# Performance work log

Hardware: AMD Instinct MI355X
Metric: run time of the kernel (lower is better)

The kernel has to match this reference:

```python
import jax, jax.numpy as jnp
import numpy as np

N = 100000      # nodes
E = 3200000     # edges (avg degree 32)
NODE, EDGE, H = 11, 2, 32
EPS = 1e-5


def setup_inputs() -> dict:
    key = jax.random.key(0)
    ks = jax.random.split(key, 12)
    def w(k, shape):  # small init like torch Linear
        return jax.random.normal(k, shape, dtype=jnp.float32) * 0.1
    inp = {
        'x': jax.random.normal(ks[0], (N, NODE), dtype=jnp.float32),
        'edge_attr': jax.random.normal(ks[1], (E, EDGE), dtype=jnp.float32),
        'edge_index': jax.random.randint(ks[2], (2, E), 0, N),
        # mlp1: Lin(13,32)-BN-ReLU-Lin(32,32)-BN-ReLU
        'w1a': w(ks[3], (NODE + EDGE, H)), 'b1a': jnp.zeros(H), 'g1a': jnp.ones(H), 'be1a': jnp.zeros(H),
        'w1b': w(ks[4], (H, H)),           'b1b': jnp.zeros(H), 'g1b': jnp.ones(H), 'be1b': jnp.zeros(H),
        # mlp2: Lin(43,32)-BN-ReLU then Lin(32,1)-ReLU (no BN on last)
        'w2a': w(ks[5], (NODE + H, H)), 'b2a': jnp.zeros(H), 'g2a': jnp.ones(H), 'be2a': jnp.zeros(H),
        'w2b': w(ks[6], (H, 1)),        'b2b': jnp.zeros(1),
        # power: Lin(11,32)-BN-ReLU-Lin(32,1)-BN-ReLU
        'wpa': w(ks[7], (NODE, H)), 'bpa': jnp.zeros(H), 'gpa': jnp.ones(H), 'bepa': jnp.zeros(H),
        'wpb': w(ks[8], (H, 1)),    'bpb': jnp.zeros(1), 'gpb': jnp.ones(1), 'bepb': jnp.zeros(1),
    }
    return inp


def _bn(x, g, b):
    # training-mode BatchNorm1d (batch stats, biased variance), like torch default
    mu = x.mean(0, keepdims=True)
    var = ((x - mu) ** 2).mean(0, keepdims=True)
    return (x - mu) * jax.lax.rsqrt(var + EPS) * g + b


def _conv(x, edge_index, edge_attr,
          w1a, b1a, g1a, be1a, w1b, b1b, g1b, be1b,
          w2a, b2a, g2a, be2a, w2b, b2b):
    src, dst = edge_index[0], edge_index[1]
    # message: cat([x_j, edge_attr]) -> mlp1
    m = jnp.concatenate([x[src], edge_attr], axis=1)          # [E, 13]
    m = jax.nn.relu(_bn(m @ w1a + b1a, g1a, be1a))            # [E, 32]
    m = jax.nn.relu(_bn(m @ w1b + b1b, g1b, be1b))            # [E, 32]
    # aggr='max' scatter to destination nodes
    agg = jax.ops.segment_max(m, dst, num_segments=x.shape[0])
    agg = jnp.where(jnp.isneginf(agg), 0.0, agg)              # empty segments -> 0
    # update: cat([x, aggr_out]) -> mlp2, then replace last feature column
    h = jax.nn.relu(_bn(jnp.concatenate([x, agg], axis=1) @ w2a + b2a, g2a, be2a))
    comb = jax.nn.relu(h @ w2b + b2b)                         # [N, 1]
    return jnp.concatenate([x[:, :-1], comb], axis=1)         # [N, 11]


def reference(x, edge_attr, edge_index,
              w1a, b1a, g1a, be1a, w1b, b1b, g1b, be1b,
              w2a, b2a, g2a, be2a, w2b, b2b,
              wpa, bpa, gpa, bepa, wpb, bpb, gpb, bepb):
    for _ in range(3):
        x = _conv(x, edge_index, edge_attr,
                  w1a, b1a, g1a, be1a, w1b, b1b, g1b, be1b,
                  w2a, b2a, g2a, be2a, w2b, b2b)
    h = jax.nn.relu(_bn(x @ wpa + bpa, gpa, bepa))
    out = jax.nn.relu(_bn(h @ wpb + bpb, gpb, bepb))
    return out
```

## Files before the change

kernel.cpp:

```cpp
#include <hip/hip_runtime.h>
#include <hip/hip_bf16.h>
#include <cstddef>

#define NN 100000
#define EE 3200000
#define NBIN 64
static const float EF = 3200000.0f;


__device__ __forceinline__ float wsum(float v) {
  #pragma unroll
  for (int off = 32; off > 0; off >>= 1) v += __shfl_down(v, off, 64);
  return v;
}

__device__ __forceinline__ void reduce64(float sum[32], float ssq[32], float* red,
                                         float* __restrict__ gsum, float* __restrict__ gssq) {
  const int wid = threadIdx.x >> 6, lane = threadIdx.x & 63;
  #pragma unroll
  for (int j = 0; j < 32; j++) {
    float a = wsum(sum[j]);
    float b = wsum(ssq[j]);
    if (lane == 0) { red[wid * 64 + j] = a; red[wid * 64 + 32 + j] = b; }
  }
  __syncthreads();
  if (threadIdx.x < 64) {
    float t = red[threadIdx.x] + red[64 + threadIdx.x] + red[128 + threadIdx.x] + red[192 + threadIdx.x];
    if (threadIdx.x < 32) unsafeAtomicAdd(&gsum[threadIdx.x], t);
    else                  unsafeAtomicAdd(&gssq[threadIdx.x - 32], t);
  }
}

__device__ __forceinline__ void loadrow(const float* __restrict__ xp, int s, float in[13]) {
  const float4* xr = reinterpret_cast<const float4*>(xp + (size_t)s * 12);
  float4 r0 = xr[0], r1 = xr[1], r2 = xr[2];
  in[0]=r0.x; in[1]=r0.y; in[2]=r0.z; in[3]=r0.w; in[4]=r1.x; in[5]=r1.y; in[6]=r1.z; in[7]=r1.w;
  in[8]=r2.x; in[9]=r2.y; in[10]=r2.z;
}


__global__ __launch_bounds__(256) void k_wprep(const float* __restrict__ w1b,
    const float* __restrict__ b1b, const float* __restrict__ g1b,
    const float* __restrict__ w2a, const float* __restrict__ b2a,
    const float* __restrict__ wpa, const float* __restrict__ bpa,
    float* __restrict__ w2tf, float* __restrict__ b1bf,
    float* __restrict__ w2aT, float* __restrict__ wpaT) {
  int t = threadIdx.x;
  for (int i = t; i < 1024; i += 256) {
    int j = i >> 5, k = i & 31;
    float d = (g1b[j] >= 0.f) ? 1.f : -1.f;
    w2tf[j * 32 + k] = d * w1b[k * 32 + j];
  }
  for (int i = t; i < 32 * 43; i += 256) { int j = i & 31, k = i >> 5; w2aT[j * 44 + k] = w2a[k * 32 + j]; }
  for (int i = t; i < 32 * 11; i += 256) { int j = i & 31, k = i >> 5; wpaT[j * 12 + k] = wpa[k * 32 + j]; }
  if (t < 32) {
    float d = (g1b[t] >= 0.f) ? 1.f : -1.f;
    b1bf[t] = d * b1b[t];
    w2aT[t * 44 + 43] = b2a[t];
    wpaT[t * 12 + 11] = bpa[t];
  }
}

__global__ __launch_bounds__(256) void k_prep(const int* __restrict__ dst, const int* __restrict__ src,
    const float* __restrict__ ea, int* __restrict__ cnt, int* __restrict__ rank,
    float* __restrict__ nsd, float* __restrict__ cmom) {
  float p0 = 0, p1 = 0, p2 = 0, p3 = 0, p4 = 0;
  const int S = gridDim.x * 256;
  for (int g = blockIdx.x * 256 + threadIdx.x; g < EE / 4; g += S) {
    int4 d4 = reinterpret_cast<const int4*>(dst)[g];
    int4 s4 = reinterpret_cast<const int4*>(src)[g];
    float4 e0 = reinterpret_cast<const float4*>(ea)[2 * g];
    float4 e1 = reinterpret_cast<const float4*>(ea)[2 * g + 1];
    int r0 = atomicAdd(&cnt[d4.x], 1);
    int r1 = atomicAdd(&cnt[d4.y], 1);
    int r2 = atomicAdd(&cnt[d4.z], 1);
    int r3 = atomicAdd(&cnt[d4.w], 1);
    reinterpret_cast<int4*>(rank)[g] = make_int4(r0, r1, r2, r3);
    atomicAdd(reinterpret_cast<int*>(&nsd[4 * s4.x]), 1);
    unsafeAtomicAdd(&nsd[4 * s4.x + 1], e0.x); unsafeAtomicAdd(&nsd[4 * s4.x + 2], e0.y);
    atomicAdd(reinterpret_cast<int*>(&nsd[4 * s4.y]), 1);
    unsafeAtomicAdd(&nsd[4 * s4.y + 1], e0.z); unsafeAtomicAdd(&nsd[4 * s4.y + 2], e0.w);
    atomicAdd(reinterpret_cast<int*>(&nsd[4 * s4.z]), 1);
    unsafeAtomicAdd(&nsd[4 * s4.z + 1], e1.x); unsafeAtomicAdd(&nsd[4 * s4.z + 2], e1.y);
    atomicAdd(reinterpret_cast<int*>(&nsd[4 * s4.w]), 1);
    unsafeAtomicAdd(&nsd[4 * s4.w + 1], e1.z); unsafeAtomicAdd(&nsd[4 * s4.w + 2], e1.w);
    p0 += e0.x * e0.x + e0.z * e0.z + e1.x * e1.x + e1.z * e1.z;
    p1 += e0.x * e0.y + e0.z * e0.w + e1.x * e1.y + e1.z * e1.w;
    p2 += e0.y * e0.y + e0.w * e0.w + e1.y * e1.y + e1.w * e1.w;
    p3 += e0.x + e0.z + e1.x + e1.z;
    p4 += e0.y + e0.w + e1.y + e1.w;
  }
  p0 = wsum(p0); p1 = wsum(p1); p2 = wsum(p2); p3 = wsum(p3); p4 = wsum(p4);
  if ((threadIdx.x & 63) == 0) {
    unsafeAtomicAdd(&cmom[0], p0); unsafeAtomicAdd(&cmom[1], p1); unsafeAtomicAdd(&cmom[2], p2);
    unsafeAtomicAdd(&cmom[3], p3); unsafeAtomicAdd(&cmom[4], p4);
  }
}

__global__ __launch_bounds__(1024) void k_scan(const int* __restrict__ cnt,
                                               int* __restrict__ starts) {
  __shared__ int part[1024];
  const int T = 1024, CH = (NN + T - 1) / T;
  int t = threadIdx.x;
  int lo = t * CH, hi = min(lo + CH, NN);
  int s = 0;
  for (int i = lo; i < hi; i++) s += cnt[i];
  part[t] = s; __syncthreads();
  for (int off = 1; off < T; off <<= 1) {
    int v = (t >= off) ? part[t - off] : 0;
    __syncthreads();
    part[t] += v;
    __syncthreads();
  }
  int run = part[t] - s;
  for (int i = lo; i < hi; i++) { starts[i] = run; run += cnt[i]; }
  if (t == T - 1) starts[NN] = EE;
}

__global__ __launch_bounds__(256) void k_scatter(const int* __restrict__ dst, const int* __restrict__ src,
    const float* __restrict__ ea, const int* __restrict__ starts, const int* __restrict__ rank,
    int4* __restrict__ edg) {
  const int S = gridDim.x * 256;
  for (int g = blockIdx.x * 256 + threadIdx.x; g < EE / 4; g += S) {
    int4 d4 = reinterpret_cast<const int4*>(dst)[g];
    int4 s4 = reinterpret_cast<const int4*>(src)[g];
    int4 r4 = reinterpret_cast<const int4*>(rank)[g];
    float4 e0 = reinterpret_cast<const float4*>(ea)[2 * g];
    float4 e1 = reinterpret_cast<const float4*>(ea)[2 * g + 1];
    edg[starts[d4.x] + r4.x] = make_int4(s4.x, __float_as_int(e0.x), __float_as_int(e0.y), 0);
    edg[starts[d4.y] + r4.y] = make_int4(s4.y, __float_as_int(e0.z), __float_as_int(e0.w), 0);
    edg[starts[d4.z] + r4.z] = make_int4(s4.z, __float_as_int(e1.x), __float_as_int(e1.y), 0);
    edg[starts[d4.w] + r4.w] = make_int4(s4.w, __float_as_int(e1.z), __float_as_int(e1.w), 0);
  }
}

__global__ __launch_bounds__(256) void k_xp(const float* __restrict__ x, float* __restrict__ xp) {
  int n = blockIdx.x * 256 + threadIdx.x;
  if (n >= NN) return;
  float v[11];
  #pragma unroll
  for (int k = 0; k < 11; k++) v[k] = x[(size_t)n * 11 + k];
  float4* o = reinterpret_cast<float4*>(xp + (size_t)n * 12);
  o[0] = make_float4(v[0], v[1], v[2], v[3]);
  o[1] = make_float4(v[4], v[5], v[6], v[7]);
  o[2] = make_float4(v[8], v[9], v[10], 0.f);
}

__global__ __launch_bounds__(256) void k_mom(const float* __restrict__ xp, const float* __restrict__ nsd,
                                             float* __restrict__ mom) {
  const int n = blockIdx.x * 256 + threadIdx.x;
  const int lane = threadIdx.x & 63;
  float v[11]; float w = 0.f; float sx = 0.f, sy = 0.f;
  #pragma unroll
  for (int k = 0; k < 11; k++) v[k] = 0.f;
  if (n < NN) {
    float4 nv = reinterpret_cast<const float4*>(nsd)[n];
    w = (float)__float_as_int(nv.x);
    sx = nv.y; sy = nv.z;
    loadrow(xp, n, v);
  }
  int ch = 0;
  #pragma unroll
  for (int a = 0; a < 11; a++) {
    float r = wsum(w * v[a]);
    if (lane == 0) unsafeAtomicAdd(&mom[ch], r);
    ch++;
  }
  #pragma unroll
  for (int a = 0; a < 11; a++) {
    #pragma unroll
    for (int b = a; b < 11; b++) {
      float r = wsum(w * v[a] * v[b]);
      if (lane == 0) unsafeAtomicAdd(&mom[ch], r);
      ch++;
    }
  }
  #pragma unroll
  for (int a = 0; a < 11; a++) {
    float rx = wsum(v[a] * sx);
    if (lane == 0) unsafeAtomicAdd(&mom[ch], rx);
    ch++;
    float ry = wsum(v[a] * sy);
    if (lane == 0) unsafeAtomicAdd(&mom[ch], ry);
    ch++;
  }
}

__device__ __forceinline__ float msym(const float* mom, const float* cmom, int k, int l) {
  int a = min(k, l), b = max(k, l);
  if (b < 11) return mom[11 + a * 11 - a * (a - 1) / 2 + (b - a)];
  if (a < 11) return mom[77 + a * 2 + (b - 11)];
  return cmom[(a - 11) + (b - 11)];
}

__global__ void k_fin1(float* __restrict__ mom, const float* __restrict__ cmom,
    const float* __restrict__ w1a, const float* __restrict__ b1a,
    const float* __restrict__ g1a, const float* __restrict__ be1a,
    float* __restrict__ w1f, float* __restrict__ wexy) {
  int j = threadIdx.x;
  float w[13], S[13];
  #pragma unroll
  for (int k = 0; k < 13; k++) w[k] = w1a[k * 32 + j];
  #pragma unroll
  for (int k = 0; k < 11; k++) S[k] = mom[k];
  S[11] = cmom[3]; S[12] = cmom[4];
  float lin = 0.f;
  #pragma unroll
  for (int k = 0; k < 13; k++) lin = fmaf(w[k], S[k], lin);
  float quad = 0.f;
  #pragma unroll
  for (int k = 0; k < 13; k++)
    #pragma unroll
    for (int l = 0; l < 13; l++) quad = fmaf(w[k] * w[l], msym(mom, cmom, k, l), quad);
  const float invE = 1.f / EF;
  float b = b1a[j];
  float mean = fmaf(lin, invE, b);
  float ey2 = (quad + 2.f * b * lin) * invE + b * b;
  float var = fmaxf(ey2 - mean * mean, 0.f);
  float A = g1a[j] * rsqrtf(var + 1e-5f);
  float C = be1a[j] - mean * A;
  #pragma unroll
  for (int k = 0; k < 13; k++) w1f[j * 16 + k] = A * w[k];
  w1f[j * 16 + 13] = fmaf(A, b, C);
  w1f[j * 16 + 14] = 0.f; w1f[j * 16 + 15] = 0.f;
  wexy[j] = A * w[11];
  wexy[32 + j] = A * w[12];
  __syncthreads();
  for (int i = j; i < 128; i += 32) mom[i] = 0.f;
}

__global__ __launch_bounds__(256) void k_P(const float* __restrict__ xp, const float* __restrict__ w1f,
                                           float* __restrict__ P) {
  const int n = blockIdx.x * 256 + threadIdx.x;
  if (n >= NN) return;
  float xv[11];
  loadrow(xp, n, xv);
  float4* op = reinterpret_cast<float4*>(P + (size_t)n * 32);
  #pragma unroll
  for (int jj = 0; jj < 8; jj++) {
    float o[4];
    #pragma unroll
    for (int u = 0; u < 4; u++) {
      int j = 4 * jj + u;
      const float* wr = w1f + j * 16;
      float acc = wr[13];
      #pragma unroll
      for (int k = 0; k < 11; k++) acc = fmaf(xv[k], wr[k], acc);
      o[u] = acc;
    }
    op[jj] = make_float4(o[0], o[1], o[2], o[3]);
  }
}

__global__ __launch_bounds__(256, 6) void k_fusedagg(
    const int* __restrict__ starts, const int4* __restrict__ edg,
    const float* __restrict__ P, const float* __restrict__ wexy,
    const float* __restrict__ w2tf, const float* __restrict__ b1bf,
    float* __restrict__ tzb, float* __restrict__ gms, float* __restrict__ gzq) {
  __shared__ float smx[4][2][32];
  __shared__ float redm[4][32], redq[4][32];
  const int tid = threadIdx.x;
  const int wid = tid >> 6, lane = tid & 63;
  const int half = lane >> 5, j = lane & 31;
  const int n = blockIdx.x * 8 + wid * 2 + half;
  const float wex = wexy[j], wey = wexy[32 + j], bz = b1bf[j];
  const float4* wc = reinterpret_cast<const float4*>(w2tf + (size_t)j * 32);
  const float4 wv0 = wc[0], wv1 = wc[1], wv2 = wc[2], wv3 = wc[3];
  const float4 wv4 = wc[4], wv5 = wc[5], wv6 = wc[6], wv7 = wc[7];
  float tz = -3.0e38f, zq = 0.f, ms = 0.f;
  int lo = 0, hi = 0;
  if (n < NN) { lo = starts[n]; hi = starts[n + 1]; }
  float* msl = &smx[wid][half][0];
  int sl = lo;
  int4 eA = make_int4(0, 0, 0, 0), eB = make_int4(0, 0, 0, 0);
  float pA = 0.f;
  if (sl < hi) {
    eA = edg[sl];
    pA = P[(size_t)eA.x * 32 + j];
  }
  if (sl + 1 < hi) eB = edg[sl + 1];
  while (sl < hi) {
    int4 eC = eB;
    if (sl + 2 < hi) eC = edg[sl + 2];
    float pN = pA;
    if (sl + 1 < hi) pN = P[(size_t)eB.x * 32 + j];
    const float ex = __int_as_float(eA.y), ey = __int_as_float(eA.z);
    const float m = fmaxf(0.f, fmaf(ex, wex, fmaf(ey, wey, pA)));
    ms += m;
    msl[j] = m;
    __builtin_amdgcn_wave_barrier();
    const float4 m0 = *reinterpret_cast<const float4*>(msl + 0);
    const float4 m1 = *reinterpret_cast<const float4*>(msl + 4);
    const float4 m2 = *reinterpret_cast<const float4*>(msl + 8);
    const float4 m3 = *reinterpret_cast<const float4*>(msl + 12);
    const float4 m4 = *reinterpret_cast<const float4*>(msl + 16);
    const float4 m5 = *reinterpret_cast<const float4*>(msl + 20);
    const float4 m6 = *reinterpret_cast<const float4*>(msl + 24);
    const float4 m7 = *reinterpret_cast<const float4*>(msl + 28);
    __builtin_amdgcn_wave_barrier();
    float z0 = bz, z1 = 0.f, z2 = 0.f, z3 = 0.f;
    z0 = fmaf(m0.x, wv0.x, z0); z1 = fmaf(m0.y, wv0.y, z1);
    z2 = fmaf(m0.z, wv0.z, z2); z3 = fmaf(m0.w, wv0.w, z3);
    z0 = fmaf(m1.x, wv1.x, z0); z1 = fmaf(m1.y, wv1.y, z1);
    z2 = fmaf(m1.z, wv1.z, z2); z3 = fmaf(m1.w, wv1.w, z3);
    z0 = fmaf(m2.x, wv2.x, z0); z1 = fmaf(m2.y, wv2.y, z1);
    z2 = fmaf(m2.z, wv2.z, z2); z3 = fmaf(m2.w, wv2.w, z3);
    z0 = fmaf(m3.x, wv3.x, z0); z1 = fmaf(m3.y, wv3.y, z1);
    z2 = fmaf(m3.z, wv3.z, z2); z3 = fmaf(m3.w, wv3.w, z3);
    z0 = fmaf(m4.x, wv4.x, z0); z1 = fmaf(m4.y, wv4.y, z1);
    z2 = fmaf(m4.z, wv4.z, z2); z3 = fmaf(m4.w, wv4.w, z3);
    z0 = fmaf(m5.x, wv5.x, z0); z1 = fmaf(m5.y, wv5.y, z1);
    z2 = fmaf(m5.z, wv5.z, z2); z3 = fmaf(m5.w, wv5.w, z3);
    z0 = fmaf(m6.x, wv6.x, z0); z1 = fmaf(m6.y, wv6.y, z1);
    z2 = fmaf(m6.z, wv6.z, z2); z3 = fmaf(m6.w, wv6.w, z3);
    z0 = fmaf(m7.x, wv7.x, z0); z1 = fmaf(m7.y, wv7.y, z1);
    z2 = fmaf(m7.z, wv7.z, z2); z3 = fmaf(m7.w, wv7.w, z3);
    const float z = (z0 + z1) + (z2 + z3);
    tz = fmaxf(tz, z);
    zq = fmaf(z, z, zq);
    eA = eB; eB = eC; pA = pN;
    ++sl;
  }
  if (n < NN) tzb[(size_t)n * 32 + j] = tz;
  float msT = ms + __shfl_xor(ms, 32, 64);
  float zqT = zq + __shfl_xor(zq, 32, 64);
  if (lane < 32) { redm[wid][j] = msT; redq[wid][j] = zqT; }
  __syncthreads();
  if (tid < 32) {
    float a = redm[0][tid] + redm[1][tid] + redm[2][tid] + redm[3][tid];
    float b = redq[0][tid] + redq[1][tid] + redq[2][tid] + redq[3][tid];
    const int bin = blockIdx.x & (NBIN - 1);
    unsafeAtomicAdd(&gms[bin * 32 + tid], a);
    unsafeAtomicAdd(&gzq[bin * 32 + tid], b);
  }
}

__global__ void k_fin2(float* __restrict__ gms, float* __restrict__ gzq,
    const float* __restrict__ w1b, const float* __restrict__ b1b,
    const float* __restrict__ g1b, const float* __restrict__ be1b,
    float* __restrict__ A2d, float* __restrict__ C2) {
  __shared__ float sm[32];
  int j = threadIdx.x;
  float msj = 0.f, zqj = 0.f;
  for (int b = 0; b < NBIN; b++) { msj += gms[b * 32 + j]; zqj += gzq[b * 32 + j]; }
  sm[j] = msj;
  __syncthreads();
  float zs = EF * b1b[j];
  #pragma unroll
  for (int k = 0; k < 32; k++) zs = fmaf(w1b[k * 32 + j], sm[k], zs);
  const float invE = 1.f / EF;
  float mu = zs * invE;
  float var = fmaxf(zqj * invE - mu * mu, 0.f);
  float A = g1b[j] * rsqrtf(var + 1e-5f);
  float C = be1b[j] - mu * A;
  float d = (g1b[j] >= 0.f) ? 1.f : -1.f;
  A2d[j] = A * d; C2[j] = C;
  for (int b = 0; b < NBIN; b++) { gms[b * 32 + j] = 0.f; gzq[b * 32 + j] = 0.f; }
}

__global__ void k_finalize(float* __restrict__ sum, float* __restrict__ ssq,
                           const float* __restrict__ g, const float* __restrict__ be,
                           float inv_n, int ncols, float* __restrict__ a, float* __restrict__ c) {
  int j = threadIdx.x;
  if (j < ncols) {
    float mu = sum[j] * inv_n;
    float var = fmaxf(ssq[j] * inv_n - mu * mu, 0.f);
    float s = rsqrtf(var + 1e-5f) * g[j];
    a[j] = s; c[j] = be[j] - mu * s;
    sum[j] = 0.f; ssq[j] = 0.f;
  }
}


__global__ __launch_bounds__(256) void k_hpre2(const float* __restrict__ xp,
    const float* __restrict__ tzb, const int* __restrict__ starts,
    const float* __restrict__ A2d, const float* __restrict__ C2, const float* __restrict__ w2aT,
    float* __restrict__ hpre, float* __restrict__ gsum, float* __restrict__ gssq) {
  __shared__ float red[256];
  const int n = blockIdx.x * 256 + threadIdx.x;
  float h[32], hh[32];
  #pragma unroll
  for (int j = 0; j < 32; j++) h[j] = 0.f;
  if (n < NN) {
    float xv[11];
    loadrow(xp, n, xv);
    const int dg = starts[n + 1] - starts[n];
    float av[32];
    if (dg > 0) {
      const float4* tp = reinterpret_cast<const float4*>(tzb + (size_t)n * 32);
      #pragma unroll
      for (int j = 0; j < 8; j++) {
        float4 v = tp[j];
        av[4 * j]     = fmaxf(0.f, fmaf(A2d[4 * j],     v.x, C2[4 * j]));
        av[4 * j + 1] = fmaxf(0.f, fmaf(A2d[4 * j + 1], v.y, C2[4 * j + 1]));
        av[4 * j + 2] = fmaxf(0.f, fmaf(A2d[4 * j + 2], v.z, C2[4 * j + 2]));
        av[4 * j + 3] = fmaxf(0.f, fmaf(A2d[4 * j + 3], v.w, C2[4 * j + 3]));
      }
    } else {
      #pragma unroll
      for (int j = 0; j < 32; j++) av[j] = 0.f;
    }
    #pragma unroll
    for (int j = 0; j < 32; j++) {
      const float* wr = w2aT + j * 44;
      float acc = wr[43];
      #pragma unroll
      for (int k = 0; k < 11; k++) acc = fmaf(xv[k], wr[k], acc);
      #pragma unroll
      for (int k = 0; k < 32; k++) acc = fmaf(av[k], wr[11 + k], acc);
      h[j] = acc;
    }
    float4* hp = reinterpret_cast<float4*>(hpre + (size_t)n * 32);
    #pragma unroll
    for (int j = 0; j < 8; j++)
      hp[j] = make_float4(h[4 * j], h[4 * j + 1], h[4 * j + 2], h[4 * j + 3]);
  }
  #pragma unroll
  for (int j = 0; j < 32; j++) hh[j] = h[j] * h[j];
  reduce64(h, hh, red, gsum, gssq);
}

__global__ __launch_bounds__(256) void k_comb(const float* __restrict__ hpre,
    const float* __restrict__ a3, const float* __restrict__ c3,
    const float* __restrict__ w2b, const float* __restrict__ b2b, float* __restrict__ xp) {
  const int n = blockIdx.x * 256 + threadIdx.x;
  if (n >= NN) return;
  const float4* hp = reinterpret_cast<const float4*>(hpre + (size_t)n * 32);
  float acc = b2b[0];
  #pragma unroll
  for (int j = 0; j < 8; j++) {
    float4 v = hp[j];
    acc += fmaxf(0.f, fmaf(v.x, a3[4 * j],     c3[4 * j]))     * w2b[4 * j];
    acc += fmaxf(0.f, fmaf(v.y, a3[4 * j + 1], c3[4 * j + 1])) * w2b[4 * j + 1];
    acc += fmaxf(0.f, fmaf(v.z, a3[4 * j + 2], c3[4 * j + 2])) * w2b[4 * j + 2];
    acc += fmaxf(0.f, fmaf(v.w, a3[4 * j + 3], c3[4 * j + 3])) * w2b[4 * j + 3];
  }
  xp[(size_t)n * 12 + 10] = fmaxf(acc, 0.f);
}


__global__ __launch_bounds__(256) void k_p5(const float* __restrict__ xp, const float* __restrict__ wpaT,
                                            float* __restrict__ ybuf,
                                            float* __restrict__ gsum, float* __restrict__ gssq) {
  __shared__ float red[256];
  const int n = blockIdx.x * 256 + threadIdx.x;
  float y[32], yy[32];
  #pragma unroll
  for (int j = 0; j < 32; j++) y[j] = 0.f;
  if (n < NN) {
    float xv[11];
    loadrow(xp, n, xv);
    #pragma unroll
    for (int j = 0; j < 32; j++) {
      const float* wr = wpaT + j * 12;
      float acc = wr[11];
      #pragma unroll
      for (int k = 0; k < 11; k++) acc = fmaf(xv[k], wr[k], acc);
      y[j] = acc;
    }
    float4* yp = reinterpret_cast<float4*>(ybuf + (size_t)n * 32);
    #pragma unroll
    for (int j = 0; j < 8; j++)
      yp[j] = make_float4(y[4 * j], y[4 * j + 1], y[4 * j + 2], y[4 * j + 3]);
  }
  #pragma unroll
  for (int j = 0; j < 32; j++) yy[j] = y[j] * y[j];
  reduce64(y, yy, red, gsum, gssq);
}

__global__ __launch_bounds__(256) void k_p6(const float* __restrict__ ybuf,
    const float* __restrict__ a4, const float* __restrict__ c4,
    const float* __restrict__ wpb, const float* __restrict__ bpb,
    float* __restrict__ yq, float* __restrict__ gsum, float* __restrict__ gssq) {
  __shared__ float red[8];
  const int n = blockIdx.x * 256 + threadIdx.x;
  float sum = 0.f, ssq = 0.f;
  if (n < NN) {
    const float4* yp = reinterpret_cast<const float4*>(ybuf + (size_t)n * 32);
    float q = bpb[0];
    #pragma unroll
    for (int j = 0; j < 8; j++) {
      float4 v = yp[j];
      q = fmaf(fmaxf(0.f, fmaf(v.x, a4[4 * j],     c4[4 * j])),     wpb[4 * j],     q);
      q = fmaf(fmaxf(0.f, fmaf(v.y, a4[4 * j + 1], c4[4 * j + 1])), wpb[4 * j + 1], q);
      q = fmaf(fmaxf(0.f, fmaf(v.z, a4[4 * j + 2], c4[4 * j + 2])), wpb[4 * j + 2], q);
      q = fmaf(fmaxf(0.f, fmaf(v.w, a4[4 * j + 3], c4[4 * j + 3])), wpb[4 * j + 3], q);
    }
    yq[n] = q;
    sum = q; ssq = q * q;
  }
  float s = wsum(sum), qq = wsum(ssq);
  const int wid = threadIdx.x >> 6, lane = threadIdx.x & 63;
  if (lane == 0) { red[wid] = s; red[4 + wid] = qq; }
  __syncthreads();
  if (threadIdx.x == 0) {
    unsafeAtomicAdd(&gsum[0], red[0] + red[1] + red[2] + red[3]);
    unsafeAtomicAdd(&gssq[0], red[4] + red[5] + red[6] + red[7]);
  }
}

__global__ __launch_bounds__(256) void k_p7(const float* __restrict__ yq,
    const float* __restrict__ a5, const float* __restrict__ c5, float* __restrict__ out) {
  int n = blockIdx.x * 256 + threadIdx.x;
  if (n < NN) out[n] = fmaxf(0.f, fmaf(yq[n], a5[0], c5[0]));
}


extern "C" void kernel_launch(void* const* d_in, const int* in_sizes, int n_in,
                              void* d_out, int out_size, void* d_ws, size_t ws_size,
                              hipStream_t stream) {
  const float* x    = (const float*)d_in[0];
  const float* ea   = (const float*)d_in[1];
  const int*   ei   = (const int*)d_in[2];
  const int*   srcp = ei;
  const int*   dstp = ei + EE;
  const float* w1a = (const float*)d_in[3],  *b1a = (const float*)d_in[4];
  const float* g1a = (const float*)d_in[5],  *be1a = (const float*)d_in[6];
  const float* w1b = (const float*)d_in[7],  *b1b = (const float*)d_in[8];
  const float* g1b = (const float*)d_in[9],  *be1b = (const float*)d_in[10];
  const float* w2a = (const float*)d_in[11], *b2a = (const float*)d_in[12];
  const float* g2a = (const float*)d_in[13], *be2a = (const float*)d_in[14];
  const float* w2b = (const float*)d_in[15], *b2b = (const float*)d_in[16];
  const float* wpa = (const float*)d_in[17], *bpa = (const float*)d_in[18];
  const float* gpa = (const float*)d_in[19], *bepa = (const float*)d_in[20];
  const float* wpb = (const float*)d_in[21], *bpb = (const float*)d_in[22];
  const float* gpb = (const float*)d_in[23], *bepb = (const float*)d_in[24];

  size_t off = 0;
  char* base = (char*)d_ws;
  auto alloc = [&](size_t bytes) -> void* {
    void* p = base + off;
    off += (bytes + 255) & ~(size_t)255;
    return p;
  };
  float* stats = (float*)alloc(2048);
  float* coef  = (float*)alloc(2048);
  float* mom   = (float*)alloc(512);
  float* cmom  = (float*)alloc(256);
  float* gmsB  = (float*)alloc(NBIN * 32 * 4);
  float* gzqB  = (float*)alloc(NBIN * 32 * 4);
  float* w1f   = (float*)alloc(16 * 32 * 4);
  float* wexy  = (float*)alloc(64 * 4);
  float* w2tf  = (float*)alloc(32 * 32 * 4);
  float* b1bf  = (float*)alloc(256);
  float* w2aT  = (float*)alloc(32 * 44 * 4);
  float* wpaT  = (float*)alloc(32 * 12 * 4);
  int*   cnt    = (int*)alloc(NN * 4);
  float* nsd    = (float*)alloc((size_t)NN * 4 * 4);
  int*   starts = (int*)alloc((NN + 1) * 4);
  int*   rank   = (int*)alloc((size_t)EE * 4);
  int4*  edg    = (int4*)alloc((size_t)EE * 16);
  float* xp     = (float*)alloc((size_t)NN * 12 * 4);
  float* P      = (float*)alloc((size_t)NN * 32 * 4);
  float* tzb    = (float*)alloc((size_t)NN * 32 * 4);
  float* hpre   = (float*)alloc((size_t)NN * 32 * 4);
  float* yq     = (float*)alloc(NN * 4);

  float *SUM3 = stats + 64,  *SSQ3 = stats + 96;
  float *SUM4 = stats + 128, *SSQ4 = stats + 160;
  float *SUM5 = stats + 192, *SSQ5 = stats + 224;
  float *A2d = coef,       *C2 = coef + 32;
  float *A3  = coef + 64,  *C3 = coef + 96;
  float *A4  = coef + 128, *C4 = coef + 160;
  float *A5  = coef + 192, *C5 = coef + 224;

  hipMemsetAsync(stats, 0, 2048, stream);
  hipMemsetAsync(mom, 0, 512 + 256, stream);
  hipMemsetAsync(gmsB, 0, NBIN * 32 * 4 * 2, stream);
  hipMemsetAsync(cnt, 0, NN * 4, stream);
  hipMemsetAsync(nsd, 0, (size_t)NN * 4 * 4, stream);

  const int GN = (NN + 255) / 256;
  const int GW = NN / 8;
  const int GE4 = (EE / 4 + 255) / 256;

  k_wprep  <<<1, 256, 0, stream>>>(w1b, b1b, g1b, w2a, b2a, wpa, bpa, w2tf, b1bf, w2aT, wpaT);
  k_prep   <<<GE4, 256, 0, stream>>>(dstp, srcp, ea, cnt, rank, nsd, cmom);
  k_scan   <<<1, 1024, 0, stream>>>(cnt, starts);
  k_scatter<<<GE4, 256, 0, stream>>>(dstp, srcp, ea, starts, rank, edg);
  k_xp     <<<GN, 256, 0, stream>>>(x, xp);

  const float invN = 1.f / (float)NN;
  for (int c = 0; c < 3; c++) {
    k_mom     <<<GN, 256, 0, stream>>>(xp, nsd, mom);
    k_fin1    <<<1, 32, 0, stream>>>(mom, cmom, w1a, b1a, g1a, be1a, w1f, wexy);
    k_P       <<<GN, 256, 0, stream>>>(xp, w1f, P);
    k_fusedagg<<<GW, 256, 0, stream>>>(starts, edg, P, wexy, w2tf, b1bf, tzb, gmsB, gzqB);
    k_fin2    <<<1, 32, 0, stream>>>(gmsB, gzqB, w1b, b1b, g1b, be1b, A2d, C2);
    k_hpre2   <<<GN, 256, 0, stream>>>(xp, tzb, starts, A2d, C2, w2aT, hpre, SUM3, SSQ3);
    k_finalize<<<1, 32, 0, stream>>>(SUM3, SSQ3, g2a, be2a, invN, 32, A3, C3);
    k_comb    <<<GN, 256, 0, stream>>>(hpre, A3, C3, w2b, b2b, xp);
  }

  k_p5      <<<GN, 256, 0, stream>>>(xp, wpaT, hpre, SUM4, SSQ4);
  k_finalize<<<1, 32, 0, stream>>>(SUM4, SSQ4, gpa, bepa, invN, 32, A4, C4);
  k_p6      <<<GN, 256, 0, stream>>>(hpre, A4, C4, wpb, bpb, yq, SUM5, SSQ5);
  k_finalize<<<1, 32, 0, stream>>>(SUM5, SSQ5, gpb, bepb, invN, 1, A5, C5);
  k_p7      <<<GN, 256, 0, stream>>>(yq, A5, C5, (float*)d_out);
}
```

Before: 4.215 ms.

## Pack per-source edge stats into one 64-bit atomic and split agg matvec across half-lanes

Replaces three separate per-edge atomics (degree count plus two float sums) with a single 64-bit integer atomic that packs degree and fixed-point quantized edge-attribute sums, then decodes them in k_mom. This cuts atomic traffic in k_prep but introduces quantization error and a bit-field overflow risk if sums exceed 27 bits. In the aggregation kernel, each lane now reads only 16 of the 32 message values from LDS and computes two half dot products, combined via a cross-lane shuffle. This halves LDS reads per edge at the cost of an extra shuffle and select.

```diff
diff --git a/kernel.cpp b/kernel.cpp
--- a/kernel.cpp
+++ b/kernel.cpp
@@ -36,6 +36,12 @@
   float4 r0 = xr[0], r1 = xr[1], r2 = xr[2];
   in[0]=r0.x; in[1]=r0.y; in[2]=r0.z; in[3]=r0.w; in[4]=r1.x; in[5]=r1.y; in[6]=r1.z; in[7]=r1.w;
   in[8]=r2.x; in[9]=r2.y; in[10]=r2.z;
+}
+
+__device__ __forceinline__ unsigned long long packsea(float x, float y) {
+  unsigned int xq = (unsigned int)(fmaf(x, 16384.f, 131072.f) + 0.5f);
+  unsigned int yq = (unsigned int)(fmaf(y, 16384.f, 131072.f) + 0.5f);
+  return (1ULL << 54) | ((unsigned long long)yq << 27) | (unsigned long long)xq;
 }
 
 
@@ -63,7 +69,7 @@
 
 __global__ __launch_bounds__(256) void k_prep(const int* __restrict__ dst, const int* __restrict__ src,
     const float* __restrict__ ea, int* __restrict__ cnt, int* __restrict__ rank,
-    float* __restrict__ nsd, float* __restrict__ cmom) {
+    unsigned long long* __restrict__ nsd, float* __restrict__ cmom) {
   float p0 = 0, p1 = 0, p2 = 0, p3 = 0, p4 = 0;
   const int S = gridDim.x * 256;
   for (int g = blockIdx.x * 256 + threadIdx.x; g < EE / 4; g += S) {
@@ -76,14 +82,10 @@
     int r2 = atomicAdd(&cnt[d4.z], 1);
     int r3 = atomicAdd(&cnt[d4.w], 1);
     reinterpret_cast<int4*>(rank)[g] = make_int4(r0, r1, r2, r3);
-    atomicAdd(reinterpret_cast<int*>(&nsd[4 * s4.x]), 1);
-    unsafeAtomicAdd(&nsd[4 * s4.x + 1], e0.x); unsafeAtomicAdd(&nsd[4 * s4.x + 2], e0.y);
-    atomicAdd(reinterpret_cast<int*>(&nsd[4 * s4.y]), 1);
-    unsafeAtomicAdd(&nsd[4 * s4.y + 1], e0.z); unsafeAtomicAdd(&nsd[4 * s4.y + 2], e0.w);
-    atomicAdd(reinterpret_cast<int*>(&nsd[4 * s4.z]), 1);
-    unsafeAtomicAdd(&nsd[4 * s4.z + 1], e1.x); unsafeAtomicAdd(&nsd[4 * s4.z + 2], e1.y);
-    atomicAdd(reinterpret_cast<int*>(&nsd[4 * s4.w]), 1);
-    unsafeAtomicAdd(&nsd[4 * s4.w + 1], e1.z); unsafeAtomicAdd(&nsd[4 * s4.w + 2], e1.w);
+    atomicAdd(&nsd[s4.x], packsea(e0.x, e0.y));
+    atomicAdd(&nsd[s4.y], packsea(e0.z, e0.w));
+    atomicAdd(&nsd[s4.z], packsea(e1.x, e1.y));
+    atomicAdd(&nsd[s4.w], packsea(e1.z, e1.w));
     p0 += e0.x * e0.x + e0.z * e0.z + e1.x * e1.x + e1.z * e1.z;
     p1 += e0.x * e0.y + e0.z * e0.w + e1.x * e1.y + e1.z * e1.w;
     p2 += e0.y * e0.y + e0.w * e0.w + e1.y * e1.y + e1.w * e1.w;
@@ -146,7 +148,8 @@
   o[2] = make_float4(v[8], v[9], v[10], 0.f);
 }
 
-__global__ __launch_bounds__(256) void k_mom(const float* __restrict__ xp, const float* __restrict__ nsd,
+__global__ __launch_bounds__(256) void k_mom(const float* __restrict__ xp,
+                                             const unsigned long long* __restrict__ nsd,
                                              float* __restrict__ mom) {
   const int n = blockIdx.x * 256 + threadIdx.x;
   const int lane = threadIdx.x & 63;
@@ -154,9 +157,13 @@
   #pragma unroll
   for (int k = 0; k < 11; k++) v[k] = 0.f;
   if (n < NN) {
-    float4 nv = reinterpret_cast<const float4*>(nsd)[n];
-    w = (float)__float_as_int(nv.x);
-    sx = nv.y; sy = nv.z;
+    unsigned long long pv = nsd[n];
+    float dg = (float)(unsigned int)(pv >> 54);
+    float sxf = (float)(unsigned int)(pv & 0x7FFFFFFull);
+    float syf = (float)(unsigned int)((pv >> 27) & 0x7FFFFFFull);
+    w = dg;
+    sx = sxf * (1.f / 16384.f) - 8.f * dg;
+    sy = syf * (1.f / 16384.f) - 8.f * dg;
     loadrow(xp, n, v);
   }
   int ch = 0;
@@ -261,70 +268,73 @@
   __shared__ float redm[4][32], redq[4][32];
   const int tid = threadIdx.x;
   const int wid = tid >> 6, lane = tid & 63;
-  const int half = lane >> 5, j = lane & 31;
+  const int half = lane >> 5, l = lane & 31;
+  const int c0 = l & 15, h = (l >> 4) & 1;
   const int n = blockIdx.x * 8 + wid * 2 + half;
-  const float wex = wexy[j], wey = wexy[32 + j], bz = b1bf[j];
-  const float4* wc = reinterpret_cast<const float4*>(w2tf + (size_t)j * 32);
-  const float4 wv0 = wc[0], wv1 = wc[1], wv2 = wc[2], wv3 = wc[3];
-  const float4 wv4 = wc[4], wv5 = wc[5], wv6 = wc[6], wv7 = wc[7];
+  const float wex = wexy[l], wey = wexy[32 + l], bz = b1bf[l];
+  const float4* wcA = reinterpret_cast<const float4*>(w2tf + (size_t)c0 * 32 + 16 * h);
+  const float4* wcB = reinterpret_cast<const float4*>(w2tf + (size_t)(c0 + 16) * 32 + 16 * h);
+  const float4 a0 = wcA[0], a1 = wcA[1], a2 = wcA[2], a3 = wcA[3];
+  const float4 b0 = wcB[0], b1 = wcB[1], b2 = wcB[2], b3 = wcB[3];
   float tz = -3.0e38f, zq = 0.f, ms = 0.f;
   int lo = 0, hi = 0;
   if (n < NN) { lo = starts[n]; hi = starts[n + 1]; }
   float* msl = &smx[wid][half][0];
+  const float* mrd = msl + 16 * h;
   int sl = lo;
   int4 eA = make_int4(0, 0, 0, 0), eB = make_int4(0, 0, 0, 0);
   float pA = 0.f;
   if (sl < hi) {
     eA = edg[sl];
-    pA = P[(size_t)eA.x * 32 + j];
+    pA = P[(size_t)eA.x * 32 + l];
   }
   if (sl + 1 < hi) eB = edg[sl + 1];
   while (sl < hi) {
     int4 eC = eB;
     if (sl + 2 < hi) eC = edg[sl + 2];
     float pN = pA;
-    if (sl + 1 < hi) pN = P[(size_t)eB.x * 32 + j];
+    if (sl + 1 < hi) pN = P[(size_t)eB.x * 32 + l];
     const float ex = __int_as_float(eA.y), ey = __int_as_float(eA.z);
     const float m = fmaxf(0.f, fmaf(ex, wex, fmaf(ey, wey, pA)));
     ms += m;
-    msl[j] = m;
+    msl[l] = m;
     __builtin_amdgcn_wave_barrier();
-    const float4 m0 = *reinterpret_cast<const float4*>(msl + 0);
-    const float4 m1 = *reinterpret_cast<const float4*>(msl + 4);
-    const float4 m2 = *reinterpret_cast<const float4*>(msl + 8);
-    const float4 m3 = *reinterpret_cast<const float4*>(msl + 12);
-    const float4 m4 = *reinterpret_cast<const float4*>(msl + 16);
-    const float4 m5 = *reinterpret_cast<const float4*>(msl + 20);
-    const float4 m6 = *reinterpret_cast<const float4*>(msl + 24);
-    const float4 m7 = *reinterpret_cast<const float4*>(msl + 28);
+    const float4 m0 = *reinterpret_cast<const float4*>(mrd + 0);
+    const float4 m1 = *reinterpret_cast<const float4*>(mrd + 4);
+    const float4 m2 = *reinterpret_cast<const float4*>(mrd + 8);
+    const float4 m3 = *reinterpret_cast<const float4*>(mrd + 12);
     __builtin_amdgcn_wave_barrier();
-    float z0 = bz, z1 = 0.f, z2 = 0.f, z3 = 0.f;
-    z0 = fmaf(m0.x, wv0.x, z0); z1 = fmaf(m0.y, wv0.y, z1);
-    z2 = fmaf(m0.z, wv0.z, z2); z3 = fmaf(m0.w, wv0.w, z3);
-    z0 = fmaf(m1.x, wv1.x, z0); z1 = fmaf(m1.y, wv1.y, z1);
-    z2 = fmaf(m1.z, wv1.z, z2); z3 = fmaf(m1.w, wv1.w, z3);
-    z0 = fmaf(m2.x, wv2.x, z0); z1 = fmaf(m2.y, wv2.y, z1);
-    z2 = fmaf(m2.z, wv2.z, z2); z3 = fmaf(m2.w, wv2.w, z3);
-    z0 = fmaf(m3.x, wv3.x, z0); z1 = fmaf(m3.y, wv3.y, z1);
-    z2 = fmaf(m3.z, wv3.z, z2); z3 = fmaf(m3.w, wv3.w, z3);
-    z0 = fmaf(m4.x, wv4.x, z0); z1 = fmaf(m4.y, wv4.y, z1);
-    z2 = fmaf(m4.z, wv4.z, z2); z3 = fmaf(m4.w, wv4.w, z3);
-    z0 = fmaf(m5.x, wv5.x, z0); z1 = fmaf(m5.y, wv5.y, z1);
-    z2 = fmaf(m5.z, wv5.z, z2); z3 = fmaf(m5.w, wv5.w, z3);
-    z0 = fmaf(m6.x, wv6.x, z0); z1 = fmaf(m6.y, wv6.y, z1);
-    z2 = fmaf(m6.z, wv6.z, z2); z3 = fmaf(m6.w, wv6.w, z3);
-    z0 = fmaf(m7.x, wv7.x, z0); z1 = fmaf(m7.y, wv7.y, z1);
-    z2 = fmaf(m7.z, wv7.z, z2); z3 = fmaf(m7.w, wv7.w, z3);
-    const float z = (z0 + z1) + (z2 + z3);
+    float zA0 = 0.f, zA1 = 0.f, zB0 = 0.f, zB1 = 0.f;
+    zA0 = fmaf(m0.x, a0.x, zA0); zA1 = fmaf(m0.y, a0.y, zA1);
+    zA0 = fmaf(m0.z, a0.z, zA0); zA1 = fmaf(m0.w, a0.w, zA1);
+    zA0 = fmaf(m1.x, a1.x, zA0); zA1 = fmaf(m1.y, a1.y, zA1);
+    zA0 = fmaf(m1.z, a1.z, zA0); zA1 = fmaf(m1.w, a1.w, zA1);
+    zA0 = fmaf(m2.x, a2.x, zA0); zA1 = fmaf(m2.y, a2.y, zA1);
+    zA0 = fmaf(m2.z, a2.z, zA0); zA1 = fmaf(m2.w, a2.w, zA1);
+    zA0 = fmaf(m3.x, a3.x, zA0); zA1 = fmaf(m3.y, a3.y, zA1);
+    zA0 = fmaf(m3.z, a3.z, zA0); zA1 = fmaf(m3.w, a3.w, zA1);
+    zB0 = fmaf(m0.x, b0.x, zB0); zB1 = fmaf(m0.y, b0.y, zB1);
+    zB0 = fmaf(m0.z, b0.z, zB0); zB1 = fmaf(m0.w, b0.w, zB1);
+    zB0 = fmaf(m1.x, b1.x, zB0); zB1 = fmaf(m1.y, b1.y, zB1);
+    zB0 = fmaf(m1.z, b1.z, zB0); zB1 = fmaf(m1.w, b1.w, zB1);
+    zB0 = fmaf(m2.x, b2.x, zB0); zB1 = fmaf(m2.y, b2.y, zB1);
+    zB0 = fmaf(m2.z, b2.z, zB0); zB1 = fmaf(m2.w, b2.w, zB1);
+    zB0 = fmaf(m3.x, b3.x, zB0); zB1 = fmaf(m3.y, b3.y, zB1);
+    zB0 = fmaf(m3.z, b3.z, zB0); zB1 = fmaf(m3.w, b3.w, zB1);
+    float pAh = zA0 + zA1;
+    float pBh = zB0 + zB1;
+    pAh += __shfl_xor(pAh, 16, 64);
+    pBh += __shfl_xor(pBh, 16, 64);
+    const float z = ((l & 16) ? pBh : pAh) + bz;
     tz = fmaxf(tz, z);
     zq = fmaf(z, z, zq);
     eA = eB; eB = eC; pA = pN;
     ++sl;
   }
-  if (n < NN) tzb[(size_t)n * 32 + j] = tz;
+  if (n < NN) tzb[(size_t)n * 32 + l] = tz;
   float msT = ms + __shfl_xor(ms, 32, 64);
   float zqT = zq + __shfl_xor(zq, 32, 64);
-  if (lane < 32) { redm[wid][j] = msT; redq[wid][j] = zqT; }
+  if (lane < 32) { redm[wid][l] = msT; redq[wid][l] = zqT; }
   __syncthreads();
   if (tid < 32) {
     float a = redm[0][tid] + redm[1][tid] + redm[2][tid] + redm[3][tid];
@@ -546,7 +556,7 @@
   float* w2aT  = (float*)alloc(32 * 44 * 4);
   float* wpaT  = (float*)alloc(32 * 12 * 4);
   int*   cnt    = (int*)alloc(NN * 4);
-  float* nsd    = (float*)alloc((size_t)NN * 4 * 4);
+  unsigned long long* nsd = (unsigned long long*)alloc((size_t)NN * 8);
   int*   starts = (int*)alloc((NN + 1) * 4);
   int*   rank   = (int*)alloc((size_t)EE * 4);
   int4*  edg    = (int4*)alloc((size_t)EE * 16);
@@ -568,7 +578,7 @@
   hipMemsetAsync(mom, 0, 512 + 256, stream);
   hipMemsetAsync(gmsB, 0, NBIN * 32 * 4 * 2, stream);
   hipMemsetAsync(cnt, 0, NN * 4, stream);
-  hipMemsetAsync(nsd, 0, (size_t)NN * 4 * 4, stream);
+  hipMemsetAsync(nsd, 0, (size_t)NN * 8, stream);
 
   const int GN = (NN + 255) / 256;
   const int GW = NN / 8;
```

Result: faster. 3.969 ms (-5.8%).
